# Optimization experiments

Measured on AMD Instinct MI355X. Metric: run time of the kernel, lower is better.

## Reference

```python
import jax, jax.numpy as jnp
import numpy as np

D = 1024
H = 16
DH = D // H


def setup_inputs() -> dict:
    key = jax.random.key(0)
    ks = jax.random.split(key, 9)
    s = 1.0 / np.sqrt(D)
    x = jax.random.normal(ks[0], (4, 2048, D), dtype=jnp.float32)
    Wq = jax.random.uniform(ks[1], (D, D), jnp.float32, -s, s)
    bq = jax.random.uniform(ks[2], (D,), jnp.float32, -s, s)
    Wk = jax.random.uniform(ks[3], (D, D), jnp.float32, -s, s)
    bk = jax.random.uniform(ks[4], (D,), jnp.float32, -s, s)
    Wv = jax.random.uniform(ks[5], (D, D), jnp.float32, -s, s)
    bv = jax.random.uniform(ks[6], (D,), jnp.float32, -s, s)
    Wo = jax.random.uniform(ks[7], (D, D), jnp.float32, -s, s)
    bo = jax.random.uniform(ks[8], (D,), jnp.float32, -s, s)
    return {"x": x, "Wq": Wq, "bq": bq, "Wk": Wk, "bk": bk,
            "Wv": Wv, "bv": bv, "Wo": Wo, "bo": bo}


def _split_heads(t):
    b, s, d = t.shape
    return t.reshape(b, s, H, DH).transpose(0, 2, 1, 3)  # (B,H,S,Dh)


def reference(x, Wq, bq, Wk, bk, Wv, bv, Wo, bo):
    # Self-attention: context = x
    q = _split_heads(x @ Wq.T + bq)
    k = _split_heads(x @ Wk.T + bk)
    v = _split_heads(x @ Wv.T + bv)
    scale = 1.0 / np.sqrt(DH).astype(np.float32)
    logits = jnp.einsum('bhqd,bhkd->bhqk', q, k) * scale
    attn = jax.nn.softmax(logits, axis=-1)
    out_h = jnp.einsum('bhqk,bhkd->bhqd', attn, v)  # (B,H,S,Dh)
    b, h, s, dh = out_h.shape
    out = out_h.transpose(0, 2, 1, 3).reshape(b, s, h * dh)
    return out @ Wo.T + bo
```

## Files before the change

### kernel.cpp

```cpp
#include <hip/hip_runtime.h>
#include <cstdint>
#include <cstddef>

typedef unsigned short u16;
typedef __attribute__((ext_vector_type(8))) short short8;
typedef __attribute__((ext_vector_type(4))) short sv4;
typedef __attribute__((ext_vector_type(4))) float f32x4;
typedef __attribute__((ext_vector_type(2))) unsigned int u32x2;
typedef __attribute__((ext_vector_type(4))) unsigned int u32x4;

__device__ __forceinline__ u16 f2bf(float f) {
  unsigned int u = __builtin_bit_cast(unsigned int, f);
  u += 0x7FFFu + ((u >> 16) & 1u);
  return (u16)(u >> 16);
}
__device__ __forceinline__ float bf2f(u16 v) {
  return __builtin_bit_cast(float, ((unsigned int)v) << 16);
}

__device__ __forceinline__ unsigned int pk_bf16(float a, float b) {
#if defined(__HIP_DEVICE_COMPILE__) && __has_builtin(__builtin_amdgcn_cvt_pk_bf16_f32)
  typedef __attribute__((ext_vector_type(2))) __bf16 bf16x2;
  bf16x2 r = __builtin_amdgcn_cvt_pk_bf16_f32(a, b);
  return __builtin_bit_cast(unsigned int, r);
#else
  return (unsigned int)f2bf(a) | ((unsigned int)f2bf(b) << 16);
#endif
}

__device__ __forceinline__ f32x4 mfma_16x16x16_bf16(sv4 a, sv4 b, f32x4 c) {
#if defined(__HIP_DEVICE_COMPILE__)
#if __has_builtin(__builtin_amdgcn_mfma_f32_16x16x16bf16_1k)
  return __builtin_amdgcn_mfma_f32_16x16x16bf16_1k(a, b, c, 0, 0, 0);
#elif __has_builtin(__builtin_amdgcn_mfma_f32_16x16x16_bf16)
  return __builtin_amdgcn_mfma_f32_16x16x16_bf16(a, b, c, 0, 0, 0);
#else
  asm volatile("v_mfma_f32_16x16x16_bf16 %0, %1, %2, %0\n\ts_nop 7\n\ts_nop 4"
               : "+v"(c) : "v"(a), "v"(b));
  return c;
#endif
#else
  (void)a; (void)b;
  return c;
#endif
}

#define GLD_LDS(g, l) __builtin_amdgcn_global_load_lds( \
    (const __attribute__((address_space(1))) void*)(g), \
    (__attribute__((address_space(3))) void*)(l), 16, 0, 0)

#define QSCL 0.18033688011112042f

__global__ void detect_dtype(const u16* __restrict__ x, int* __restrict__ flag)
{
  const int lane = threadIdx.x;
  int hit = 0;
#pragma unroll
  for (int j = 0; j < 4; ++j) {
    float v = bf2f(x[lane * 4 + j]);
    if (!(v > -1000.f && v < 1000.f)) hit = 1;
  }
  unsigned long long any = __ballot(hit != 0);
  if (lane == 0) *flag = (any != 0ull) ? 1 : 0;
}

__global__ __launch_bounds__(256)
void convert_wb(const void* Wq, const void* Wk, const void* Wv, const void* Wo,
                const void* bq, const void* bk, const void* bv, const void* bo,
                u16* __restrict__ Wc, u16* __restrict__ bc, const int* __restrict__ flag)
{
  const int fp32 = *flag;
  const size_t base = ((size_t)blockIdx.x * 256 + threadIdx.x) * 8;
  const void* src; u16* dst; size_t local; int sel;
  if (base < (size_t)4 * 1048576) {
    sel = (int)(base >> 20);
    local = base & 1048575u;
    src = (sel == 0) ? Wq : (sel == 1) ? Wk : (sel == 2) ? Wv : Wo;
    dst = Wc + (size_t)sel * 1048576 + local;
  } else {
    const size_t rem = base - (size_t)4 * 1048576;
    sel = (int)(rem >> 10);
    local = rem & 1023u;
    src = (sel == 0) ? bq : (sel == 1) ? bk : (sel == 2) ? bv : bo;
    dst = bc + (size_t)sel * 1024 + local;
  }
  const float scale = (sel == 0) ? QSCL : 1.0f;
  if (fp32) {
    const float* s = (const float*)src + local;
    u32x4 w;
#pragma unroll
    for (int j = 0; j < 4; ++j) w[j] = pk_bf16(s[2 * j] * scale, s[2 * j + 1] * scale);
    *(short8*)dst = __builtin_bit_cast(short8, w);
  } else {
    const u16* s = (const u16*)src + local;
    if (sel == 0) {
      u32x4 w;
#pragma unroll
      for (int j = 0; j < 4; ++j)
        w[j] = pk_bf16(bf2f(s[2 * j]) * scale, bf2f(s[2 * j + 1]) * scale);
      *(short8*)dst = __builtin_bit_cast(short8, w);
    } else {
      *(short8*)dst = *(const short8*)s;
    }
  }
}

__global__ __launch_bounds__(256)
void convert_x_off(const void* __restrict__ x, u16* __restrict__ dst,
                   const int* __restrict__ flag, int b)
{
  const int fp32 = *flag;
  const size_t base = ((size_t)blockIdx.x * 256 + threadIdx.x) * 8;
  const size_t src_e = (size_t)b * 2048 * 1024 + base;
  if (fp32) {
    const float* s = (const float*)x + src_e;
    u32x4 w;
#pragma unroll
    for (int j = 0; j < 4; ++j) w[j] = pk_bf16(s[2 * j], s[2 * j + 1]);
    *(short8*)(dst + base) = __builtin_bit_cast(short8, w);
  } else {
    *(short8*)(dst + base) = *(const short8*)((const u16*)x + src_e);
  }
}

__global__ __launch_bounds__(256)
void gemm_bt(const u16* __restrict__ A,
             const u16* __restrict__ B0, const u16* __restrict__ B1, const u16* __restrict__ B2,
             const u16* __restrict__ bias, u16* __restrict__ C, int Ntot, int K)
{
  __shared__ __align__(16) u16 Alds[128 * 32];
  __shared__ __align__(16) u16 Blds[128 * 32];
  const int tid  = threadIdx.x;
  const int wave = tid >> 6, lane = tid & 63;
  const int quad = lane >> 4, l15 = lane & 15;
  const int m0  = blockIdx.x * 128;
  const int n0g = blockIdx.y * 128;
  const int sel = n0g >> 10;
  const u16* Bm = (sel == 0) ? B0 : ((sel == 1) ? B1 : B2);
  const u16* bb = bias + (size_t)sel * 1024;
  const int n0 = n0g & 1023;
  const int wr = (wave >> 1) * 64, wc = (wave & 1) * 64;

  f32x4 acc[4][4] = {};
  const int srow = lane >> 2;
  const int skc  = (lane & 3) * 8;
  const u16* Ag = A  + (size_t)(m0 + srow) * K + skc;
  const u16* Bg = Bm + (size_t)(n0 + srow) * K + skc;

  for (int kt = 0; kt < K; kt += 32) {
    __syncthreads();
#pragma unroll
    for (int t = 0; t < 2; ++t) {
      const int seg = wave * 2 + t;
      GLD_LDS(Ag + (size_t)(seg * 16) * K + kt, Alds + seg * 512);
      GLD_LDS(Bg + (size_t)(seg * 16) * K + kt, Blds + seg * 512);
    }
    __syncthreads();

    short8 af[4], bfr[4];
#pragma unroll
    for (int i = 0; i < 4; ++i)
      af[i] = *(const short8*)&Alds[(wr + i * 16 + l15) * 32 + quad * 8];
#pragma unroll
    for (int j = 0; j < 4; ++j)
      bfr[j] = *(const short8*)&Blds[(wc + j * 16 + l15) * 32 + quad * 8];
#pragma unroll
    for (int i = 0; i < 4; ++i)
#pragma unroll
      for (int j = 0; j < 4; ++j)
        acc[i][j] = __builtin_amdgcn_mfma_f32_16x16x32_bf16(af[i], bfr[j], acc[i][j], 0, 0, 0);
  }

#pragma unroll
  for (int i = 0; i < 4; ++i) {
    const int mr = m0 + wr + i * 16 + quad * 4;
#pragma unroll
    for (int j = 0; j < 4; ++j) {
      const int ncl = wc + j * 16 + l15;
      const float bvv = bf2f(bb[n0 + ncl]);
#pragma unroll
      for (int r = 0; r < 4; ++r)
        C[(size_t)(mr + r) * Ntot + n0g + ncl] = f2bf(acc[i][j][r] + bvv);
    }
  }
}

__global__ __launch_bounds__(256)
void gemm_bt_out(const u16* __restrict__ A, const u16* __restrict__ Bm,
                 const u16* __restrict__ bias, void* __restrict__ C16,
                 void* __restrict__ C32, int Ntot, int K, const int* __restrict__ flag)
{
  __shared__ __align__(16) u16 Alds[128 * 32];
  __shared__ __align__(16) u16 Blds[128 * 32];
  const int tid  = threadIdx.x;
  const int wave = tid >> 6, lane = tid & 63;
  const int quad = lane >> 4, l15 = lane & 15;
  const int m0 = blockIdx.x * 128;
  const int n0 = blockIdx.y * 128;
  const int wr = (wave >> 1) * 64, wc = (wave & 1) * 64;

  f32x4 acc[4][4] = {};
  const int srow = lane >> 2;
  const int skc  = (lane & 3) * 8;
  const u16* Ag = A  + (size_t)(m0 + srow) * K + skc;
  const u16* Bg = Bm + (size_t)(n0 + srow) * K + skc;

  for (int kt = 0; kt < K; kt += 32) {
    __syncthreads();
#pragma unroll
    for (int t = 0; t < 2; ++t) {
      const int seg = wave * 2 + t;
      GLD_LDS(Ag + (size_t)(seg * 16) * K + kt, Alds + seg * 512);
      GLD_LDS(Bg + (size_t)(seg * 16) * K + kt, Blds + seg * 512);
    }
    __syncthreads();

    short8 af[4], bfr[4];
#pragma unroll
    for (int i = 0; i < 4; ++i)
      af[i] = *(const short8*)&Alds[(wr + i * 16 + l15) * 32 + quad * 8];
#pragma unroll
    for (int j = 0; j < 4; ++j)
      bfr[j] = *(const short8*)&Blds[(wc + j * 16 + l15) * 32 + quad * 8];
#pragma unroll
    for (int i = 0; i < 4; ++i)
#pragma unroll
      for (int j = 0; j < 4; ++j)
        acc[i][j] = __builtin_amdgcn_mfma_f32_16x16x32_bf16(af[i], bfr[j], acc[i][j], 0, 0, 0);
  }

  if (*flag != 0) {
    float* Cf = (float*)C32;
#pragma unroll
    for (int i = 0; i < 4; ++i) {
      const int mr = m0 + wr + i * 16 + quad * 4;
#pragma unroll
      for (int j = 0; j < 4; ++j) {
        const int ncl = wc + j * 16 + l15;
        const float bvv = bf2f(bias[n0 + ncl]);
#pragma unroll
        for (int r = 0; r < 4; ++r)
          Cf[(size_t)(mr + r) * Ntot + n0 + ncl] = acc[i][j][r] + bvv;
      }
    }
  } else {
    u16* Cb = (u16*)C16;
#pragma unroll
    for (int i = 0; i < 4; ++i) {
      const int mr = m0 + wr + i * 16 + quad * 4;
#pragma unroll
      for (int j = 0; j < 4; ++j) {
        const int ncl = wc + j * 16 + l15;
        const float bvv = bf2f(bias[n0 + ncl]);
#pragma unroll
        for (int r = 0; r < 4; ++r)
          Cb[(size_t)(mr + r) * Ntot + n0 + ncl] = f2bf(acc[i][j][r] + bvv);
      }
    }
  }
}

__global__ __launch_bounds__(512, 4)
void attn_s(const u16* __restrict__ QKV, u16* __restrict__ O)
{
  __shared__ __align__(16) u16 Klds[64 * 72];
  __shared__ __align__(16) unsigned int Vlds[64 * 32];
  const int tid  = threadIdx.x;
  const int wave = tid >> 6, lane = tid & 63;
  const int quad = lane >> 4, l15 = lane & 15;

  const int i  = blockIdx.x;
  const int j  = i >> 3;
  const int qt = j & 7;
  const int g  = (i & 7) + ((j >> 3) << 3);
  const int h  = g & 15;
  const int z  = g >> 4;

  const u16* QKVb = QKV + (size_t)z * 2048 * 3072;
  u16* Ob = O + (size_t)z * 2048 * 1024;
  const int q0 = qt * 256;

  short8 qf[2][2];
  const u16* Qb = QKVb + (size_t)(q0 + wave * 32) * 3072 + h * 64;
#pragma unroll
  for (int rt = 0; rt < 2; ++rt)
#pragma unroll
    for (int kh = 0; kh < 2; ++kh)
      qf[rt][kh] = *(const short8*)(Qb + (size_t)(rt * 16 + l15) * 3072 + kh * 32 + quad * 8);

  f32x4 oaccT[4][2] = {};
  float lrow[2] = {};

  const int kwoff = (tid >> 3) * 72 + (tid & 7) * 8;
  const int d0v = (tid >> 5) * 4;
  const int kb  = (tid >> 1) & 15;
  const int kl  = tid & 1;

  const u16* kgp = QKVb + 1024 + h * 64 + (size_t)(tid >> 3) * 3072 + (tid & 7) * 8;
  const u16* vgp = QKVb + 2048 + h * 64 + (size_t)(2 * (tid & 31)) * 3072 + d0v;
  const size_t ADV = (size_t)64 * 3072;

  for (int kv0 = 0; kv0 < 2048; kv0 += 64) {
    __syncthreads();
    {
      *(short8*)&Klds[kwoff] = *(const short8*)kgp;
      const sv4 v0 = *(const sv4*)vgp;
      const sv4 v1 = *(const sv4*)(vgp + 3072);
#pragma unroll
      for (int jj = 0; jj < 4; ++jj) {
        const int d = d0v + jj;
        Vlds[d * 32 + ((kb ^ (d & 15)) << 1) + kl] =
            ((unsigned int)(unsigned short)v0[jj]) |
            (((unsigned int)(unsigned short)v1[jj]) << 16);
      }
      kgp += ADV; vgp += ADV;
    }
    __syncthreads();

    f32x4 sacc[4][2] = {};
#pragma unroll
    for (int kh = 0; kh < 2; ++kh) {
      short8 kf[4];
#pragma unroll
      for (int ct = 0; ct < 4; ++ct)
        kf[ct] = *(const short8*)&Klds[(ct * 16 + l15) * 72 + kh * 32 + quad * 8];
      __builtin_amdgcn_s_setprio(1);
#pragma unroll
      for (int ct = 0; ct < 4; ++ct)
#pragma unroll
        for (int rt = 0; rt < 2; ++rt)
          sacc[ct][rt] = __builtin_amdgcn_mfma_f32_16x16x32_bf16(kf[ct], qf[rt][kh], sacc[ct][rt], 0, 0, 0);
      __builtin_amdgcn_s_setprio(0);
    }

    sv4 p16[4][2];
#pragma unroll
    for (int rt = 0; rt < 2; ++rt) {
      float rs = 0.f;
#pragma unroll
      for (int ct = 0; ct < 4; ++ct) {
        float p0 = __builtin_amdgcn_exp2f(sacc[ct][rt][0]);
        float p1 = __builtin_amdgcn_exp2f(sacc[ct][rt][1]);
        float p2 = __builtin_amdgcn_exp2f(sacc[ct][rt][2]);
        float p3 = __builtin_amdgcn_exp2f(sacc[ct][rt][3]);
        rs += (p0 + p1) + (p2 + p3);
        u32x2 pw;
        pw[0] = pk_bf16(p0, p1);
        pw[1] = pk_bf16(p2, p3);
        p16[ct][rt] = __builtin_bit_cast(sv4, pw);
      }
      rs += __shfl_xor(rs, 16, 64);
      rs += __shfl_xor(rs, 32, 64);
      lrow[rt] += rs;
    }

    __builtin_amdgcn_s_setprio(1);
#pragma unroll
    for (int ct = 0; ct < 4; ++ct) {
#pragma unroll
      for (int dt = 0; dt < 4; ++dt) {
        const int d = dt * 16 + l15;
        const int idx = d * 32 + (((ct * 4 + quad) ^ (d & 15)) << 1);
        const sv4 vfr = *(const sv4*)&Vlds[idx];
#pragma unroll
        for (int rt = 0; rt < 2; ++rt)
          oaccT[dt][rt] = mfma_16x16x16_bf16(vfr, p16[ct][rt], oaccT[dt][rt]);
      }
    }
    __builtin_amdgcn_s_setprio(0);
  }

#pragma unroll
  for (int rt = 0; rt < 2; ++rt) {
    const float inv = 1.f / lrow[rt];
    u16* Op = Ob + (size_t)(q0 + wave * 32 + rt * 16 + l15) * 1024 + h * 64;
#pragma unroll
    for (int dt = 0; dt < 4; ++dt) {
      u32x2 ow;
      ow[0] = pk_bf16(oaccT[dt][rt][0] * inv, oaccT[dt][rt][1] * inv);
      ow[1] = pk_bf16(oaccT[dt][rt][2] * inv, oaccT[dt][rt][3] * inv);
      *(sv4*)(Op + dt * 16 + quad * 4) = __builtin_bit_cast(sv4, ow);
    }
  }
}

extern "C" void kernel_launch(void* const* d_in, const int* in_sizes, int n_in,
                              void* d_out, int out_size, void* d_ws, size_t ws_size,
                              hipStream_t stream)
{
  int* flag = (int*)d_ws;
  u16* Wc   = (u16*)((char*)d_ws + 256);
  u16* bc   = Wc + (size_t)4 * 1048576;
  char* after_wb = (char*)(bc + 4096);

  detect_dtype<<<1, 64, 0, stream>>>((const u16*)d_in[0], flag);
  convert_wb<<<2050, 256, 0, stream>>>(d_in[1], d_in[3], d_in[5], d_in[7],
                                       d_in[2], d_in[4], d_in[6], d_in[8],
                                       Wc, bc, flag);

  const size_t need_batched =
      (size_t)(after_wb - (char*)d_ws) + ((size_t)8192 * 3072 + (size_t)8192 * 1024) * 2;

  if (ws_size >= need_batched) {
    u16* QKV = (u16*)after_wb;
    u16* xO  = QKV + (size_t)8192 * 3072;

    convert_x_off<<<4096, 256, 0, stream>>>(d_in[0], xO, flag, 0);
    gemm_bt<<<dim3(64, 24), 256, 0, stream>>>(xO, Wc, Wc + 1048576, Wc + 2097152,
                                              bc, QKV, 3072, 1024);
    attn_s<<<512, 512, 0, stream>>>(QKV, xO);
    gemm_bt_out<<<dim3(64, 8), 256, 0, stream>>>(xO, Wc + (size_t)3 * 1048576,
                                                 bc + 3 * 1024, d_out, d_out,
                                                 1024, 1024, flag);
  } else {
    u16* xc   = (u16*)after_wb;
    u16* QKVb = xc + (size_t)2048 * 1024;
    u16* Obb  = QKVb + (size_t)2048 * 3072;
    for (int b = 0; b < 4; ++b) {
      convert_x_off<<<1024, 256, 0, stream>>>(d_in[0], xc, flag, b);
      gemm_bt<<<dim3(16, 24), 256, 0, stream>>>(xc, Wc, Wc + 1048576, Wc + 2097152,
                                                bc, QKVb, 3072, 1024);
      attn_s<<<128, 512, 0, stream>>>(QKVb, Obb);
      void* outb16 = (void*)((char*)d_out + (size_t)b * 2048 * 1024 * 2);
      void* outb32 = (void*)((char*)d_out + (size_t)b * 2048 * 1024 * 4);
      gemm_bt_out<<<dim3(16, 8), 256, 0, stream>>>(Obb, Wc + (size_t)3 * 1048576,
                                                   bc + 3 * 1024, outb16, outb32,
                                                   1024, 1024, flag);
    }
  }
}
```

Baseline: 305.0 us.

## Double attention KV tile to 128 and fuse QK, exp and PV per column chunk

Each loop iteration of the attention kernel now loads a 128-key block of K and V into LDS instead of 64, which halves the number of barrier pairs and loop iterations. The inner loop is restructured so that every 16-key chunk computes its scores, exponentiates them and immediately feeds them into the PV MFMAs. This keeps only a small score tile live in registers, reducing register pressure. The per-row sum cross-lane shuffles are moved out of the loop to a single reduction at the end. The cost is roughly double the LDS footprint per block, which could limit occupancy, and the finer-grained interleaving may give the scheduler less room to overlap work.

```diff
diff --git a/kernel.cpp b/kernel.cpp
--- a/kernel.cpp
+++ b/kernel.cpp
@@ -263,8 +263,8 @@
 __global__ __launch_bounds__(512, 4)
 void attn_s(const u16* __restrict__ QKV, u16* __restrict__ O)
 {
-  __shared__ __align__(16) u16 Klds[64 * 72];
-  __shared__ __align__(16) unsigned int Vlds[64 * 32];
+  __shared__ __align__(16) u16 Klds[128 * 72];
+  __shared__ __align__(16) unsigned int Vlds[64 * 64];
   const int tid  = threadIdx.x;
   const int wave = tid >> 6, lane = tid & 63;
   const int quad = lane >> 4, l15 = lane & 15;
@@ -289,85 +289,93 @@
       qf[rt][kh] = *(const short8*)(Qb + (size_t)(rt * 16 + l15) * 3072 + kh * 32 + quad * 8);
 
   f32x4 oaccT[4][2] = {};
-  float lrow[2] = {};
+  float rsp[2] = {};
 
   const int kwoff = (tid >> 3) * 72 + (tid & 7) * 8;
-  const int d0v = (tid >> 5) * 4;
-  const int kb  = (tid >> 1) & 15;
-  const int kl  = tid & 1;
+  const int d0v = (tid & 15) * 4;
+  const int kb1 = tid >> 5;
+  const int kl1 = (tid >> 4) & 1;
 
   const u16* kgp = QKVb + 1024 + h * 64 + (size_t)(tid >> 3) * 3072 + (tid & 7) * 8;
-  const u16* vgp = QKVb + 2048 + h * 64 + (size_t)(2 * (tid & 31)) * 3072 + d0v;
-  const size_t ADV = (size_t)64 * 3072;
-
-  for (int kv0 = 0; kv0 < 2048; kv0 += 64) {
+  const u16* vgp = QKVb + 2048 + h * 64 + (size_t)(2 * (tid >> 4)) * 3072 + d0v;
+  const size_t ADV = (size_t)128 * 3072;
+
+  for (int kv0 = 0; kv0 < 2048; kv0 += 128) {
     __syncthreads();
     {
-      *(short8*)&Klds[kwoff] = *(const short8*)kgp;
+      *(short8*)&Klds[kwoff]           = *(const short8*)kgp;
+      *(short8*)&Klds[kwoff + 64 * 72] = *(const short8*)(kgp + (size_t)64 * 3072);
       const sv4 v0 = *(const sv4*)vgp;
       const sv4 v1 = *(const sv4*)(vgp + 3072);
+      const sv4 v2 = *(const sv4*)(vgp + (size_t)64 * 3072);
+      const sv4 v3 = *(const sv4*)(vgp + (size_t)65 * 3072);
 #pragma unroll
       for (int jj = 0; jj < 4; ++jj) {
         const int d = d0v + jj;
-        Vlds[d * 32 + ((kb ^ (d & 15)) << 1) + kl] =
+        const int bidx = d * 64 + ((kb1 ^ (d & 15)) << 1) + kl1;
+        Vlds[bidx] =
             ((unsigned int)(unsigned short)v0[jj]) |
             (((unsigned int)(unsigned short)v1[jj]) << 16);
+        Vlds[bidx + 32] =
+            ((unsigned int)(unsigned short)v2[jj]) |
+            (((unsigned int)(unsigned short)v3[jj]) << 16);
       }
       kgp += ADV; vgp += ADV;
     }
     __syncthreads();
 
-    f32x4 sacc[4][2] = {};
-#pragma unroll
-    for (int kh = 0; kh < 2; ++kh) {
-      short8 kf[4];
-#pragma unroll
-      for (int ct = 0; ct < 4; ++ct)
-        kf[ct] = *(const short8*)&Klds[(ct * 16 + l15) * 72 + kh * 32 + quad * 8];
+#pragma unroll
+    for (int ct = 0; ct < 8; ++ct) {
+      const short8 kf0 = *(const short8*)&Klds[(ct * 16 + l15) * 72 + quad * 8];
+      const short8 kf1 = *(const short8*)&Klds[(ct * 16 + l15) * 72 + 32 + quad * 8];
       __builtin_amdgcn_s_setprio(1);
-#pragma unroll
-      for (int ct = 0; ct < 4; ++ct)
-#pragma unroll
-        for (int rt = 0; rt < 2; ++rt)
-          sacc[ct][rt] = __builtin_amdgcn_mfma_f32_16x16x32_bf16(kf[ct], qf[rt][kh], sacc[ct][rt], 0, 0, 0);
+      f32x4 s0 = {}, s1 = {};
+      s0 = __builtin_amdgcn_mfma_f32_16x16x32_bf16(kf0, qf[0][0], s0, 0, 0, 0);
+      s0 = __builtin_amdgcn_mfma_f32_16x16x32_bf16(kf1, qf[0][1], s0, 0, 0, 0);
+      s1 = __builtin_amdgcn_mfma_f32_16x16x32_bf16(kf0, qf[1][0], s1, 0, 0, 0);
+      s1 = __builtin_amdgcn_mfma_f32_16x16x32_bf16(kf1, qf[1][1], s1, 0, 0, 0);
       __builtin_amdgcn_s_setprio(0);
-    }
-
-    sv4 p16[4][2];
-#pragma unroll
-    for (int rt = 0; rt < 2; ++rt) {
-      float rs = 0.f;
-#pragma unroll
-      for (int ct = 0; ct < 4; ++ct) {
-        float p0 = __builtin_amdgcn_exp2f(sacc[ct][rt][0]);
-        float p1 = __builtin_amdgcn_exp2f(sacc[ct][rt][1]);
-        float p2 = __builtin_amdgcn_exp2f(sacc[ct][rt][2]);
-        float p3 = __builtin_amdgcn_exp2f(sacc[ct][rt][3]);
-        rs += (p0 + p1) + (p2 + p3);
-        u32x2 pw;
-        pw[0] = pk_bf16(p0, p1);
-        pw[1] = pk_bf16(p2, p3);
-        p16[ct][rt] = __builtin_bit_cast(sv4, pw);
-      }
-      rs += __shfl_xor(rs, 16, 64);
-      rs += __shfl_xor(rs, 32, 64);
-      lrow[rt] += rs;
-    }
-
-    __builtin_amdgcn_s_setprio(1);
-#pragma unroll
-    for (int ct = 0; ct < 4; ++ct) {
+
+      sv4 p16[2];
+      {
+        float p0 = __builtin_amdgcn_exp2f(s0[0]);
+        float p1 = __builtin_amdgcn_exp2f(s0[1]);
+        float p2 = __builtin_amdgcn_exp2f(s0[2]);
+        float p3 = __builtin_amdgcn_exp2f(s0[3]);
+        rsp[0] += (p0 + p1) + (p2 + p3);
+        u32x2 pw; pw[0] = pk_bf16(p0, p1); pw[1] = pk_bf16(p2, p3);
+        p16[0] = __builtin_bit_cast(sv4, pw);
+      }
+      {
+        float p0 = __builtin_amdgcn_exp2f(s1[0]);
+        float p1 = __builtin_amdgcn_exp2f(s1[1]);
+        float p2 = __builtin_amdgcn_exp2f(s1[2]);
+        float p3 = __builtin_amdgcn_exp2f(s1[3]);
+        rsp[1] += (p0 + p1) + (p2 + p3);
+        u32x2 pw; pw[0] = pk_bf16(p0, p1); pw[1] = pk_bf16(p2, p3);
+        p16[1] = __builtin_bit_cast(sv4, pw);
+      }
+
+      __builtin_amdgcn_s_setprio(1);
 #pragma unroll
       for (int dt = 0; dt < 4; ++dt) {
         const int d = dt * 16 + l15;
-        const int idx = d * 32 + (((ct * 4 + quad) ^ (d & 15)) << 1);
+        const int idx = d * 64 + (((ct * 4 + quad) ^ (d & 15)) << 1);
         const sv4 vfr = *(const sv4*)&Vlds[idx];
-#pragma unroll
-        for (int rt = 0; rt < 2; ++rt)
-          oaccT[dt][rt] = mfma_16x16x16_bf16(vfr, p16[ct][rt], oaccT[dt][rt]);
-      }
-    }
-    __builtin_amdgcn_s_setprio(0);
+        oaccT[dt][0] = mfma_16x16x16_bf16(vfr, p16[0], oaccT[dt][0]);
+        oaccT[dt][1] = mfma_16x16x16_bf16(vfr, p16[1], oaccT[dt][1]);
+      }
+      __builtin_amdgcn_s_setprio(0);
+    }
+  }
+
+  float lrow[2];
+#pragma unroll
+  for (int rt = 0; rt < 2; ++rt) {
+    float rs = rsp[rt];
+    rs += __shfl_xor(rs, 16, 64);
+    rs += __shfl_xor(rs, 32, 64);
+    lrow[rt] = rs;
   }
 
 #pragma unroll
```

Result: no change. 302.6 us (-0.8%).
